# Kernel optimization log

Hardware: AMD Instinct MI355X
Metric: run time of the kernel (lower is better)

## Reference

```python
import jax, jax.numpy as jnp
import numpy as np
import math

EPS = 1e-6  # PCEN eps


def _logit(p):
    return math.log(p / (1.0 - p))


def _pcen(mel, log_s, log_alpha, log_delta, log_r, dmin, dmax):
    """PCEN: per-channel energy normalization. mel: (B, M, T); params: (M,)."""
    s = jnp.clip(jax.nn.sigmoid(log_s), 0.05, 0.3)            # (M,)
    alpha = jnp.clip(jax.nn.sigmoid(log_alpha), 0.9, 0.999)   # (M,)
    delta = jnp.clip(jnp.exp(log_delta), dmin, dmax)          # (M,)
    r = jnp.clip(jax.nn.sigmoid(log_r), 0.05, 0.25)           # (M,)

    # IIR smoother over time: smoother_0 = mel[..., 0];
    # for t in 0..T-1: smoother = (1-s)*smoother + s*mel_t  (t=0 included -> smoothed_0 = mel_0)
    mel_t = jnp.transpose(mel, (2, 0, 1))  # (T, B, M)

    def step(sm, x):
        sm = (1.0 - s) * sm + s * x
        return sm, sm

    _, smoothed_t = jax.lax.scan(step, mel_t[0], mel_t)
    smoothed = jnp.transpose(smoothed_t, (1, 2, 0))  # (B, M, T)

    gain = (EPS + smoothed) ** (-alpha[None, :, None])
    d = delta[None, :, None]
    rr = r[None, :, None]
    return (mel * gain + d) ** rr - d ** rr


def setup_inputs() -> dict:
    key = jax.random.key(0)
    B, M, T = 64, 80, 4000
    mel = jax.random.uniform(key, (B, M, T), dtype=jnp.float32)
    f = jnp.full
    return {
        "mel": mel,
        # non-stationary expert PCEN (s=0.025, alpha=0.99, delta=2.0, r=0.5)
        "log_s_ns": f((M,), _logit(0.025), jnp.float32),
        "log_alpha_ns": f((M,), _logit(0.99), jnp.float32),
        "log_delta_ns": f((M,), math.log(2.0), jnp.float32),
        "log_r_ns": f((M,), _logit(0.5), jnp.float32),
        # stationary expert PCEN (s=0.15, alpha=0.99, delta=0.01, r=0.1)
        "log_s_st": f((M,), _logit(0.15), jnp.float32),
        "log_alpha_st": f((M,), _logit(0.99), jnp.float32),
        "log_delta_st": f((M,), math.log(0.01), jnp.float32),
        "log_r_st": f((M,), _logit(0.1), jnp.float32),
        "gate_temp": jnp.asarray(5.0, jnp.float32),
    }


def reference(mel, log_s_ns, log_alpha_ns, log_delta_ns, log_r_ns,
              log_s_st, log_alpha_st, log_delta_st, log_r_st, gate_temp):
    out_ns = _pcen(mel, log_s_ns, log_alpha_ns, log_delta_ns, log_r_ns, 0.5, 5.0)
    out_st = _pcen(mel, log_s_st, log_alpha_st, log_delta_st, log_r_st, 0.001, 0.1)

    # routing signal: spectral flatness + spectral tilt (0 learnable params)
    log_mel = jnp.log(mel + 1e-8)
    geo = jnp.exp(jnp.mean(log_mel, axis=1, keepdims=True))          # (B,1,T)
    arith = jnp.mean(mel, axis=1, keepdims=True) + 1e-8
    sf = jnp.clip(geo / arith, 0.0, 1.0)

    M = mel.shape[1]
    low = jnp.mean(mel[:, : M // 3, :], axis=1, keepdims=True)
    high = jnp.mean(mel[:, 2 * M // 3 :, :], axis=1, keepdims=True)
    tilt = jnp.clip(low / (low + high + 1e-8), 0.0, 1.0)

    sf_adj = sf + (1.0 - sf) * jax.nn.relu(tilt - 0.6)
    gate = jax.nn.sigmoid(gate_temp * (sf_adj - 0.5))
    return gate * out_st + (1.0 - gate) * out_ns
```

## Files before the change

kernel.cpp:

```cpp
#include <hip/hip_runtime.h>
#include <math.h>

static constexpr int kM = 80;
static constexpr int kT = 4000;
static constexpr int kB = 64;
static constexpr int kLow = kM / 3;
static constexpr int kHighStart = 2 * kM / 3;
static constexpr int kHighCount = kM - kHighStart;
static constexpr int kTrunc = 12;
#define EPSF 1e-6f
#define LOG2E 1.4426950408889634f

typedef float vfloat4 __attribute__((ext_vector_type(4)));
typedef float vfloat2 __attribute__((ext_vector_type(2)));

__device__ __forceinline__ float hw_exp2(float x) { return __builtin_amdgcn_exp2f(x); }
__device__ __forceinline__ float hw_log2(float x) { return __builtin_amdgcn_logf(x); }

__device__ __forceinline__ float fast_sigmoid(float x) {
    return __builtin_amdgcn_rcpf(1.0f + hw_exp2(-x * LOG2E));
}

__global__ __launch_bounds__(256) void gate_kernel(
    const float* __restrict__ mel,
    const float* __restrict__ gate_temp,
    float* __restrict__ gate)
{
    const int tid = threadIdx.x;
    const int c   = tid & 127;
    const int h   = tid >> 7;
    const int b   = blockIdx.y;
    const int col = blockIdx.x * 128 + c;
    const bool valid = (col < kT);

    const float* base = mel + (size_t)b * kM * kT + col;

    float slog = 0.f, ssum = 0.f, sband = 0.f;
    if (valid) {
        if (h == 0) {
            #pragma unroll 20
            for (int m = 0; m < 40; ++m) {
                const float v = base[(size_t)m * kT];
                slog += hw_log2(v + 1e-8f);
                ssum += v;
                if (m < kLow) sband += v;
            }
        } else {
            #pragma unroll 20
            for (int m = 40; m < 80; ++m) {
                const float v = base[(size_t)m * kT];
                slog += hw_log2(v + 1e-8f);
                ssum += v;
                if (m >= kHighStart) sband += v;
            }
        }
    }

    __shared__ float p1[3][128];
    if (h == 1) {
        p1[0][c] = slog; p1[1][c] = ssum; p1[2][c] = sband;
    }
    __syncthreads();

    if (h == 0 && valid) {
        const float tlog  = slog + p1[0][c];
        const float tsum  = ssum + p1[1][c];
        const float thigh = p1[2][c];
        const float tlow  = sband;

        const float gt = gate_temp[0];
        const float geo   = hw_exp2(tlog * (1.0f / kM));
        const float arith = tsum * (1.0f / kM) + 1e-8f;
        float sf = geo * __builtin_amdgcn_rcpf(arith);
        sf = fminf(fmaxf(sf, 0.0f), 1.0f);
        const float low  = tlow  * (1.0f / kLow);
        const float high = thigh * (1.0f / kHighCount);
        float tilt = low * __builtin_amdgcn_rcpf(low + high + 1e-8f);
        tilt = fminf(fmaxf(tilt, 0.0f), 1.0f);
        const float sfa = sf + (1.0f - sf) * fmaxf(tilt - 0.6f, 0.0f);
        gate[(size_t)b * kT + col] = fast_sigmoid(gt * (sfa - 0.5f));
    }
}

__global__ __launch_bounds__(256) void pcen_kernel(
    const float* __restrict__ mel,
    const float* __restrict__ ls_ns, const float* __restrict__ la_ns,
    const float* __restrict__ ld_ns, const float* __restrict__ lr_ns,
    const float* __restrict__ ls_st, const float* __restrict__ la_st,
    const float* __restrict__ ld_st, const float* __restrict__ lr_st,
    const float* __restrict__ gate,
    float* __restrict__ out)
{
    const int m = blockIdx.x;
    const int b = blockIdx.y;

    const float s_ns     = fminf(fmaxf(fast_sigmoid(ls_ns[m]), 0.05f), 0.3f);
    const float alpha_ns = fminf(fmaxf(fast_sigmoid(la_ns[m]), 0.9f), 0.999f);
    const float delta_ns = fminf(fmaxf(hw_exp2(ld_ns[m] * LOG2E), 0.5f), 5.0f);
    const float r_ns     = fminf(fmaxf(fast_sigmoid(lr_ns[m]), 0.05f), 0.25f);
    const float s_st     = fminf(fmaxf(fast_sigmoid(ls_st[m]), 0.05f), 0.3f);
    const float alpha_st = fminf(fmaxf(fast_sigmoid(la_st[m]), 0.9f), 0.999f);
    const float alpha_dummy = alpha_st;
    const float delta_st = fminf(fmaxf(hw_exp2(ld_st[m] * LOG2E), 0.001f), 0.1f);
    const float r_st     = fminf(fmaxf(fast_sigmoid(lr_st[m]), 0.05f), 0.25f);
    const float dr_ns = hw_exp2(r_ns * hw_log2(delta_ns));
    const float dr_st = hw_exp2(r_st * hw_log2(delta_st));
    (void)alpha_dummy;

    const vfloat2 a2 = {1.0f - s_ns, 1.0f - s_st};
    const vfloat2 s2 = {s_ns, s_st};
    const vfloat2 d2 = {delta_ns, delta_st};
    const float man = -alpha_ns, mas = -alpha_st;

    const size_t rowoff = ((size_t)b * kM + m) * kT;
    const float* row = mel + rowoff;

    const int i  = threadIdx.x;
    const int t0 = i * 16;
    const bool valid = (t0 < kT);

    float x[16];
    float gv[16];
    if (valid) {
        const float4* p = reinterpret_cast<const float4*>(row + t0);
        #pragma unroll
        for (int q = 0; q < 4; ++q) {
            const float4 v = p[q];
            x[4*q+0] = v.x; x[4*q+1] = v.y; x[4*q+2] = v.z; x[4*q+3] = v.w;
        }
        const float4* gp = reinterpret_cast<const float4*>(gate + (size_t)b * kT + t0);
        #pragma unroll
        for (int q = 0; q < 4; ++q) {
            const float4 v = gp[q];
            gv[4*q+0] = v.x; gv[4*q+1] = v.y; gv[4*q+2] = v.z; gv[4*q+3] = v.w;
        }
    } else {
        #pragma unroll
        for (int k = 0; k < 16; ++k) { x[k] = 0.0f; gv[k] = 0.0f; }
    }

    __shared__ float sv0;
    if (i == 0) sv0 = x[0];

    vfloat2 Bv = {0.0f, 0.0f};
    #pragma unroll
    for (int k = 0; k < 16; ++k) {
        Bv = a2 * Bv + s2 * x[k];
    }
    const vfloat2 p2  = a2 * a2;
    const vfloat2 p4  = p2 * p2;
    const vfloat2 p8  = p4 * p4;
    const vfloat2 A2  = p8 * p8;

    __shared__ vfloat2 Btab[256];
    Btab[i] = Bv;
    __syncthreads();

    vfloat2 sm = {0.0f, 0.0f};
    vfloat2 pw = {1.0f, 1.0f};
    #pragma unroll
    for (int k = 0; k < kTrunc; ++k) {
        const vfloat2 Bk = Btab[(i - 1 - k) & 255];
        if (k < i) {
            sm = pw * Bk + sm;
            pw = pw * A2;
        }
    }
    if (i <= kTrunc) {
        const float x0 = sv0;
        const vfloat2 x02 = {x0, x0};
        sm = pw * x02 + sm;
    }

    if (valid) {
        float4* op = reinterpret_cast<float4*>(out + rowoff + t0);
        #pragma unroll
        for (int q = 0; q < 4; ++q) {
            float4 v;
            #pragma unroll
            for (int j = 0; j < 4; ++j) {
                const int k = 4*q + j;
                const float xv = x[k];
                sm = a2 * sm + s2 * xv;
                vfloat2 g2;
                g2.x = hw_exp2(man * hw_log2(sm.x + EPSF));
                g2.y = hw_exp2(mas * hw_log2(sm.y + EPSF));
                const vfloat2 u2 = g2 * xv + d2;
                const float on = hw_exp2(r_ns * hw_log2(u2.x)) - dr_ns;
                const float os = hw_exp2(r_st * hw_log2(u2.y)) - dr_st;
                (&v.x)[j] = fmaf(gv[k], os - on, on);
            }
            op[q] = v;
        }
    }
}

extern "C" void kernel_launch(void* const* d_in, const int* in_sizes, int n_in,
                              void* d_out, int out_size, void* d_ws, size_t ws_size,
                              hipStream_t stream)
{
    const float* mel       = (const float*)d_in[0];
    const float* ls_ns     = (const float*)d_in[1];
    const float* la_ns     = (const float*)d_in[2];
    const float* ld_ns     = (const float*)d_in[3];
    const float* lr_ns     = (const float*)d_in[4];
    const float* ls_st     = (const float*)d_in[5];
    const float* la_st     = (const float*)d_in[6];
    const float* ld_st     = (const float*)d_in[7];
    const float* lr_st     = (const float*)d_in[8];
    const float* gate_temp = (const float*)d_in[9];
    float* out  = (float*)d_out;
    float* gate = (float*)d_ws;

    dim3 gA((kT + 127) / 128, kB);
    gate_kernel<<<gA, 256, 0, stream>>>(mel, gate_temp, gate);

    dim3 gB(kM, kB);
    pcen_kernel<<<gB, 256, 0, stream>>>(mel, ls_ns, la_ns, ld_ns, lr_ns,
                                        ls_st, la_st, ld_st, lr_st, gate, out);
}
```

Baseline: 180.1 us.

## Split gate reduction into per-group partial sums plus finalize kernel

Replaces the single gate kernel with two kernels. The first computes partial log/sum/band sums over 16-channel groups with float4 loads, giving far more blocks. The second combines the five groups and computes the gate. This is meant to raise parallelism and memory-level concurrency in the channel reduction, at the cost of an extra launch, extra workspace traffic for the partials, and a dependency on workspace size. The old kernel stays as a fallback.

```diff
diff --git a/kernel.cpp b/kernel.cpp
--- a/kernel.cpp
+++ b/kernel.cpp
@@ -8,6 +8,10 @@
 static constexpr int kHighStart = 2 * kM / 3;
 static constexpr int kHighCount = kM - kHighStart;
 static constexpr int kTrunc = 12;
+static constexpr int kGroups = 5;
+static constexpr int kGQ = 4;
+static constexpr size_t kGateFloats = (size_t)kB * kT;
+static constexpr size_t kPartFloats = (size_t)kB * kGroups * kGQ * kT;
 #define EPSF 1e-6f
 #define LOG2E 1.4426950408889634f
 
@@ -19,6 +23,88 @@
 
 __device__ __forceinline__ float fast_sigmoid(float x) {
     return __builtin_amdgcn_rcpf(1.0f + hw_exp2(-x * LOG2E));
+}
+
+__global__ __launch_bounds__(256) void partial_kernel(
+    const float* __restrict__ mel,
+    float* __restrict__ part)
+{
+    const int tid = threadIdx.x;
+    const int tq  = blockIdx.x;
+    const int bg  = blockIdx.y;
+    const int b   = bg / kGroups;
+    const int g   = bg - b * kGroups;
+    const int t0  = tq * (kT / 4) + tid * 4;
+    const bool valid = (tid < 250);
+
+    const int m0 = g * 16;
+    vfloat4 slog = {0.f,0.f,0.f,0.f}, ssum = {0.f,0.f,0.f,0.f};
+    vfloat4 slow = {0.f,0.f,0.f,0.f}, shigh = {0.f,0.f,0.f,0.f};
+
+    if (valid) {
+        const float* base = mel + ((size_t)b * kM + m0) * kT + t0;
+        #pragma unroll
+        for (int j = 0; j < 16; ++j) {
+            const int m = m0 + j;
+            const vfloat4 v = *reinterpret_cast<const vfloat4*>(base + (size_t)j * kT);
+            vfloat4 lg;
+            lg.x = hw_log2(v.x + 1e-8f); lg.y = hw_log2(v.y + 1e-8f);
+            lg.z = hw_log2(v.z + 1e-8f); lg.w = hw_log2(v.w + 1e-8f);
+            slog += lg;
+            ssum += v;
+            if (m < kLow)        slow  += v;
+            if (m >= kHighStart) shigh += v;
+        }
+        float* pb = part + ((size_t)bg * kGQ) * kT + t0;
+        *reinterpret_cast<vfloat4*>(pb)          = slog;
+        *reinterpret_cast<vfloat4*>(pb +   kT)   = ssum;
+        *reinterpret_cast<vfloat4*>(pb + 2*kT)   = slow;
+        *reinterpret_cast<vfloat4*>(pb + 3*kT)   = shigh;
+    }
+}
+
+__global__ __launch_bounds__(256) void gate_finalize_kernel(
+    const float* __restrict__ part,
+    const float* __restrict__ gate_temp,
+    float* __restrict__ gate)
+{
+    const int tid = threadIdx.x;
+    const int tq  = blockIdx.x;
+    const int b   = blockIdx.y;
+    const int t0  = tq * (kT / 4) + tid * 4;
+    if (tid >= 250) return;
+
+    vfloat4 tlog = {0.f,0.f,0.f,0.f}, tsum = {0.f,0.f,0.f,0.f};
+    vfloat4 tlow = {0.f,0.f,0.f,0.f}, thigh = {0.f,0.f,0.f,0.f};
+    #pragma unroll
+    for (int g = 0; g < kGroups; ++g) {
+        const float* pb = part + ((size_t)(b * kGroups + g) * kGQ) * kT + t0;
+        tlog  += *reinterpret_cast<const vfloat4*>(pb);
+        tsum  += *reinterpret_cast<const vfloat4*>(pb +   kT);
+        tlow  += *reinterpret_cast<const vfloat4*>(pb + 2*kT);
+        thigh += *reinterpret_cast<const vfloat4*>(pb + 3*kT);
+    }
+
+    const float gt = gate_temp[0];
+    vfloat4 o;
+    #pragma unroll
+    for (int q = 0; q < 4; ++q) {
+        const float sl = tlog[q];
+        const float ss = tsum[q];
+        const float lo = tlow[q];
+        const float hi = thigh[q];
+        const float geo   = hw_exp2(sl * (1.0f / kM));
+        const float arith = ss * (1.0f / kM) + 1e-8f;
+        float sf = geo * __builtin_amdgcn_rcpf(arith);
+        sf = fminf(fmaxf(sf, 0.0f), 1.0f);
+        const float low  = lo * (1.0f / kLow);
+        const float high = hi * (1.0f / kHighCount);
+        float tilt = low * __builtin_amdgcn_rcpf(low + high + 1e-8f);
+        tilt = fminf(fmaxf(tilt, 0.0f), 1.0f);
+        const float sfa = sf + (1.0f - sf) * fmaxf(tilt - 0.6f, 0.0f);
+        o[q] = fast_sigmoid(gt * (sfa - 0.5f));
+    }
+    *reinterpret_cast<vfloat4*>(gate + (size_t)b * kT + t0) = o;
 }
 
 __global__ __launch_bounds__(256) void gate_kernel(
@@ -100,12 +186,10 @@
     const float r_ns     = fminf(fmaxf(fast_sigmoid(lr_ns[m]), 0.05f), 0.25f);
     const float s_st     = fminf(fmaxf(fast_sigmoid(ls_st[m]), 0.05f), 0.3f);
     const float alpha_st = fminf(fmaxf(fast_sigmoid(la_st[m]), 0.9f), 0.999f);
-    const float alpha_dummy = alpha_st;
     const float delta_st = fminf(fmaxf(hw_exp2(ld_st[m] * LOG2E), 0.001f), 0.1f);
     const float r_st     = fminf(fmaxf(fast_sigmoid(lr_st[m]), 0.05f), 0.25f);
     const float dr_ns = hw_exp2(r_ns * hw_log2(delta_ns));
     const float dr_st = hw_exp2(r_st * hw_log2(delta_st));
-    (void)alpha_dummy;
 
     const vfloat2 a2 = {1.0f - s_ns, 1.0f - s_st};
     const vfloat2 s2 = {s_ns, s_st};
@@ -212,8 +296,15 @@
     float* out  = (float*)d_out;
     float* gate = (float*)d_ws;
 
-    dim3 gA((kT + 127) / 128, kB);
-    gate_kernel<<<gA, 256, 0, stream>>>(mel, gate_temp, gate);
+    const size_t need = (kGateFloats + kPartFloats) * sizeof(float);
+    if (ws_size >= need) {
+        float* part = gate + kGateFloats;
+        partial_kernel<<<dim3(4, kB * kGroups), 256, 0, stream>>>(mel, part);
+        gate_finalize_kernel<<<dim3(4, kB), 256, 0, stream>>>(part, gate_temp, gate);
+    } else {
+        dim3 gA((kT + 127) / 128, kB);
+        gate_kernel<<<gA, 256, 0, stream>>>(mel, gate_temp, gate);
+    }
 
     dim3 gB(kM, kB);
     pcen_kernel<<<gB, 256, 0, stream>>>(mel, ls_ns, la_ns, ld_ns, lr_ns,
```

Result: slower. 191.3 us (+6.2%).
